# Optimization experiments

Measured on AMD Instinct MI355X. Metric: run time of the kernel, lower is better.

The kernel has to match this reference:

```python
import jax, jax.numpy as jnp
import numpy as np

D_MODEL = 1536
N_HEADS = 16
HEAD_DIM = D_MODEL // N_HEADS  # 96
NUM_BLOCKS = HEAD_DIM // 24    # 4


def generate_leech_kernel(dim=24):
    base = np.zeros((dim, dim), dtype=np.float32)
    for i in range(dim - 1):
        base[i, i] = 2.0
        base[i, i + 1] = 2.0
    base[-1, -1] = 2.0
    base[-1, 0] = -2.0
    q, _ = np.linalg.qr(base)
    return jnp.asarray(q.astype(np.float32))


def setup_inputs() -> dict:
    key = jax.random.key(0)
    k1, k2, k3 = jax.random.split(key, 3)
    x = jax.random.normal(k1, (2, 2048, D_MODEL), dtype=jnp.float32)
    # nn.Linear weights stored [out, in]; kept that layout, applied as x @ W.T
    w_qkv = jax.random.normal(k2, (3 * D_MODEL, D_MODEL), dtype=jnp.float32) * (D_MODEL ** -0.5)
    w_out = jax.random.normal(k3, (D_MODEL, D_MODEL), dtype=jnp.float32) * (D_MODEL ** -0.5)
    leech_kernel = generate_leech_kernel(24)
    return {"x": x, "w_qkv": w_qkv, "w_out": w_out, "leech_kernel": leech_kernel}


def _apply_kernel(t, kernel):
    # t: [b, h, s, head_dim] -> blockwise 24x24 rotation
    b, h, s, d = t.shape
    t = t.reshape(b, h, s, NUM_BLOCKS, 24)
    t = jnp.einsum('bhsni,ij->bhsnj', t, kernel)
    return t.reshape(b, h, s, d)


def reference(x, w_qkv, w_out, leech_kernel):
    bsz, steps, _ = x.shape
    qkv = x @ w_qkv.T  # [b, s, 3*d]
    qkv = qkv.reshape(bsz, steps, 3, N_HEADS, HEAD_DIM)
    qkv = jnp.transpose(qkv, (2, 0, 3, 1, 4))  # [3, b, h, s, hd]
    q, k, v = qkv[0], qkv[1], qkv[2]
    q = _apply_kernel(q, leech_kernel)
    k = _apply_kernel(k, leech_kernel)
    scale = HEAD_DIM ** -0.5
    scores = jnp.einsum('bhqd,bhkd->bhqk', q, k) * scale
    attn = jax.nn.softmax(scores, axis=-1)
    out = jnp.einsum('bhqk,bhkd->bhqd', attn, v)
    out = jnp.transpose(out, (0, 2, 1, 3)).reshape(bsz, steps, -1)
    return out @ w_out.T
```

## Files before the change

### kernel.cpp

```cpp
#include <hip/hip_runtime.h>
#include <cmath>

#define D_MODEL 1536
#define N_HEADS 16
#define HEAD_DIM 96
#define SEQ 2048
#define BATCH 2
#define M_TOTAL 4096
#define N_QKV 4608
#define QK_LOG2E 0.14724449f

typedef unsigned short ushort_t;
typedef __attribute__((ext_vector_type(8))) short bf16x8;
typedef __attribute__((ext_vector_type(4))) float f32x4;

static __device__ __forceinline__ ushort_t f2bf(float f) {
    unsigned u = __builtin_bit_cast(unsigned, f);
    u += 0x7fffu + ((u >> 16) & 1u);
    return (ushort_t)(u >> 16);
}

static __device__ __forceinline__ unsigned pk2bf(float lo, float hi) {
#if __has_builtin(__builtin_amdgcn_cvt_pk_bf16_f32)
    auto v = __builtin_amdgcn_cvt_pk_bf16_f32(lo, hi);
    return __builtin_bit_cast(unsigned, v);
#else
    return (unsigned)f2bf(lo) | ((unsigned)f2bf(hi) << 16);
#endif
}

static __device__ __forceinline__ float fast_exp2(float x) {
#if __has_builtin(__builtin_amdgcn_exp2f)
    return __builtin_amdgcn_exp2f(x);
#else
    return __expf(x * 0.69314718056f);
#endif
}

typedef const __attribute__((address_space(1))) unsigned int* gas_t;
typedef __attribute__((address_space(3))) unsigned int* las_t;
static __device__ __forceinline__ void gld_lds16(const void* g, void* l) {
    __builtin_amdgcn_global_load_lds((gas_t)g, (las_t)l, 16, 0, 0);
}

#define MFMA16(a, b, c) __builtin_amdgcn_mfma_f32_16x16x32_bf16(a, b, c, 0, 0, 0)

__global__ __launch_bounds__(256) void convert_f32_bf16(
    const float* __restrict__ in, ushort_t* __restrict__ out, int n)
{
    const int i = (blockIdx.x * 256 + threadIdx.x) * 4;
    if (i >= n) return;
    float4 v = *(const float4*)(in + i);
    ushort4 o;
    o.x = f2bf(v.x); o.y = f2bf(v.y); o.z = f2bf(v.z); o.w = f2bf(v.w);
    *(ushort4*)(out + i) = o;
}

__global__ __launch_bounds__(256) void prep_wqkv(
    const float* __restrict__ W, const float* __restrict__ Kern,
    ushort_t* __restrict__ Wb)
{
    __shared__ float Kl[576];
    const int t = threadIdx.x;
    for (int i = t; i < 576; i += 256) Kl[i] = Kern[i];
    __syncthreads();
    const int g = blockIdx.y;
    const int k = blockIdx.x * 256 + t;
    const float* src = W + (size_t)g * 24 * D_MODEL + k;
    ushort_t* dst = Wb + (size_t)g * 24 * D_MODEL + k;
    if (g < 128) {
        float in[24];
#pragma unroll
        for (int i = 0; i < 24; ++i) in[i] = src[(size_t)i * D_MODEL];
#pragma unroll
        for (int j = 0; j < 24; ++j) {
            float s = 0.f;
#pragma unroll
            for (int i = 0; i < 24; ++i) s = fmaf(in[i], Kl[i * 24 + j], s);
            dst[(size_t)j * D_MODEL] = f2bf(s);
        }
    } else {
#pragma unroll
        for (int i = 0; i < 24; ++i) dst[(size_t)i * D_MODEL] = f2bf(src[(size_t)i * D_MODEL]);
    }
}

__global__ __launch_bounds__(256, 4) void gemm_qkv_bf16(
    const ushort_t* __restrict__ X, const ushort_t* __restrict__ W,
    ushort_t* __restrict__ qb, ushort_t* __restrict__ kb, ushort_t* __restrict__ vtb)
{
    __shared__ ushort_t As[128 * 64];
    __shared__ ushort_t Bs[128 * 64];
    const int t = threadIdx.x;
    const int lane = t & 63, w = t >> 6;
    const int c = lane & 15, qd = lane >> 4;
    const int m0 = blockIdx.y * 128, n0 = blockIdx.x * 128;
    const int wr = (w >> 1) * 64, wc = (w & 1) * 64;
    const int lr = lane >> 3;
    const int lc = (lane & 7) ^ lr;
    const char* Xb = (const char*)X;
    const char* Wp = (const char*)W;
    const size_t rowb = 2 * D_MODEL;

    f32x4 acc[4][4];
#pragma unroll
    for (int i = 0; i < 4; ++i)
#pragma unroll
        for (int j = 0; j < 4; ++j) acc[i][j] = {0.f, 0.f, 0.f, 0.f};

    for (int k0 = 0; k0 < D_MODEL; k0 += 64) {
        __syncthreads();
#pragma unroll
        for (int j = 0; j < 4; ++j) {
            const int g = w * 4 + j;
            const int row = g * 8 + lr;
            gld_lds16(Xb + (size_t)(m0 + row) * rowb + k0 * 2 + lc * 16,
                      (char*)As + g * 1024);
            gld_lds16(Wp + (size_t)(n0 + row) * rowb + k0 * 2 + lc * 16,
                      (char*)Bs + g * 1024);
        }
        __syncthreads();
#pragma unroll
        for (int kc = 0; kc < 2; ++kc) {
            const int sx = ((kc * 4 + qd) ^ (c & 7)) * 16;
            bf16x8 af[4], bfr[4];
#pragma unroll
            for (int i = 0; i < 4; ++i)
                af[i] = *(const bf16x8*)((const char*)As + (wr + i * 16 + c) * 128 + sx);
#pragma unroll
            for (int j = 0; j < 4; ++j)
                bfr[j] = *(const bf16x8*)((const char*)Bs + (wc + j * 16 + c) * 128 + sx);
#pragma unroll
            for (int i = 0; i < 4; ++i)
#pragma unroll
                for (int j = 0; j < 4; ++j)
                    acc[i][j] = MFMA16(af[i], bfr[j], acc[i][j]);
        }
    }
#pragma unroll
    for (int j = 0; j < 4; ++j) {
        const int n = n0 + wc + j * 16 + c;
        const int which = n / D_MODEL;
        const int rem = n % D_MODEL;
        const int head = rem / HEAD_DIM;
        const int d = rem % HEAD_DIM;
        if (which < 2) {
            ushort_t* dst = which == 0 ? qb : kb;
            const float sc2 = which == 0 ? QK_LOG2E : 1.0f;
#pragma unroll
            for (int i = 0; i < 4; ++i)
#pragma unroll
                for (int r = 0; r < 4; ++r) {
                    const int m = m0 + wr + i * 16 + qd * 4 + r;
                    const int b_ = m >> 11, s_ = m & (SEQ - 1);
                    dst[((size_t)(b_ * N_HEADS + head) * SEQ + s_) * HEAD_DIM + d] =
                        f2bf(acc[i][j][r] * sc2);
                }
        } else {
            const int b_ = m0 >> 11;
            const int sb = (m0 & (SEQ - 1)) + wr + qd * 4;
            ushort_t* dstv = vtb + ((size_t)(b_ * N_HEADS + head) * HEAD_DIM + d) * SEQ;
#pragma unroll
            for (int i = 0; i < 4; ++i) {
                ushort4 o4;
                o4.x = f2bf(acc[i][j][0]); o4.y = f2bf(acc[i][j][1]);
                o4.z = f2bf(acc[i][j][2]); o4.w = f2bf(acc[i][j][3]);
                *(ushort4*)&dstv[sb + i * 16] = o4;
            }
        }
    }
}

__global__ __launch_bounds__(256, 4) void gemm_out_bf16(
    const ushort_t* __restrict__ A, const ushort_t* __restrict__ W,
    float* __restrict__ C)
{
    __shared__ ushort_t As[128 * 64];
    __shared__ ushort_t Bs[128 * 64];
    const int t = threadIdx.x;
    const int lane = t & 63, w = t >> 6;
    const int c = lane & 15, qd = lane >> 4;
    const int m0 = blockIdx.y * 128, n0 = blockIdx.x * 128;
    const int wr = (w >> 1) * 64, wc = (w & 1) * 64;
    const int lr = lane >> 3;
    const int lc = (lane & 7) ^ lr;
    const char* Ab = (const char*)A;
    const char* Wp = (const char*)W;
    const size_t rowb = 2 * D_MODEL;

    f32x4 acc[4][4];
#pragma unroll
    for (int i = 0; i < 4; ++i)
#pragma unroll
        for (int j = 0; j < 4; ++j) acc[i][j] = {0.f, 0.f, 0.f, 0.f};

    for (int k0 = 0; k0 < D_MODEL; k0 += 64) {
        __syncthreads();
#pragma unroll
        for (int j = 0; j < 4; ++j) {
            const int g = w * 4 + j;
            const int row = g * 8 + lr;
            gld_lds16(Ab + (size_t)(m0 + row) * rowb + k0 * 2 + lc * 16,
                      (char*)As + g * 1024);
            gld_lds16(Wp + (size_t)(n0 + row) * rowb + k0 * 2 + lc * 16,
                      (char*)Bs + g * 1024);
        }
        __syncthreads();
#pragma unroll
        for (int kc = 0; kc < 2; ++kc) {
            const int sx = ((kc * 4 + qd) ^ (c & 7)) * 16;
            bf16x8 af[4], bfr[4];
#pragma unroll
            for (int i = 0; i < 4; ++i)
                af[i] = *(const bf16x8*)((const char*)As + (wr + i * 16 + c) * 128 + sx);
#pragma unroll
            for (int j = 0; j < 4; ++j)
                bfr[j] = *(const bf16x8*)((const char*)Bs + (wc + j * 16 + c) * 128 + sx);
#pragma unroll
            for (int i = 0; i < 4; ++i)
#pragma unroll
                for (int j = 0; j < 4; ++j)
                    acc[i][j] = MFMA16(af[i], bfr[j], acc[i][j]);
        }
    }
#pragma unroll
    for (int i = 0; i < 4; ++i)
#pragma unroll
        for (int j = 0; j < 4; ++j)
#pragma unroll
            for (int r = 0; r < 4; ++r)
                C[(size_t)(m0 + wr + i * 16 + qd * 4 + r) * D_MODEL + n0 + wc + j * 16 + c] =
                    acc[i][j][r];
}

__global__ __launch_bounds__(256, 1) void flash_bf16(
    const ushort_t* __restrict__ Q, const ushort_t* __restrict__ K,
    const ushort_t* __restrict__ VT, ushort_t* __restrict__ attn)
{
    __shared__ ushort_t Ks[2][12 * 64 * 8];
    __shared__ ushort_t Vt[2][96 * 64];
    __shared__ ushort_t Ps[4][64 * 72];

    const int t = threadIdx.x;
    const int lane = t & 63, w = t >> 6;
    const int c = lane & 15, qd = lane >> 4;
    const int lr = lane >> 3;
    const int lc = (lane & 7) ^ lr;
    const int h = blockIdx.y, bb = blockIdx.z;
    const int q0 = blockIdx.x * 256;
    const size_t base = ((size_t)(bb * N_HEADS + h)) * SEQ * HEAD_DIM;
    const ushort_t* Qb = Q + base;
    const char* Kb = (const char*)(K + base);
    const ushort_t* VTb = VT + base;

    bf16x8 aq[4][3];
#pragma unroll
    for (int qi = 0; qi < 4; ++qi)
#pragma unroll
        for (int kc = 0; kc < 3; ++kc)
            aq[qi][kc] = *(const bf16x8*)(Qb +
                (size_t)(q0 + w * 64 + qi * 16 + c) * HEAD_DIM + kc * 32 + qd * 8);

    f32x4 oacc[6][4];
#pragma unroll
    for (int jd = 0; jd < 6; ++jd)
#pragma unroll
        for (int qi = 0; qi < 4; ++qi) oacc[jd][qi] = {0.f, 0.f, 0.f, 0.f};
    float lrow[4] = {0.f, 0.f, 0.f, 0.f};

    const int g0 = w * 3;
#define ISSUE_STAGE(buf, ktv)                                                   \
    {                                                                           \
        const char* kp = Kb + (size_t)(ktv) * 64 * 192;                         \
        _Pragma("unroll")                                                       \
        for (int jj = 0; jj < 3; ++jj) {                                        \
            const int g = g0 + jj;                                              \
            gld_lds16(kp + (size_t)lane * 192 + g * 16, (char*)Ks[buf] + g * 1024); \
        }                                                                       \
        _Pragma("unroll")                                                       \
        for (int jj = 0; jj < 3; ++jj) {                                        \
            const int g = g0 + jj;                                              \
            const int d = g * 8 + lr;                                           \
            gld_lds16((const char*)(VTb + (size_t)d * SEQ + (ktv) * 64 + lc * 8), \
                      (char*)Vt[buf] + g * 1024);                               \
        }                                                                       \
    }

    ISSUE_STAGE(0, 0)

    for (int kt = 0; kt < SEQ / 64; ++kt) {
        const int cur = kt & 1;
        __syncthreads();
        if (kt + 1 < SEQ / 64) ISSUE_STAGE(cur ^ 1, kt + 1)

        f32x4 sacc[4][4];
#pragma unroll
        for (int kti = 0; kti < 4; ++kti)
#pragma unroll
            for (int qi = 0; qi < 4; ++qi) sacc[kti][qi] = {0.f, 0.f, 0.f, 0.f};
#pragma unroll
        for (int kc = 0; kc < 3; ++kc) {
            bf16x8 ak[4];
#pragma unroll
            for (int kti = 0; kti < 4; ++kti)
                ak[kti] = *(const bf16x8*)&Ks[cur][((kc * 4 + qd) * 64 + kti * 16 + c) * 8];
#pragma unroll
            for (int kti = 0; kti < 4; ++kti)
#pragma unroll
                for (int qi = 0; qi < 4; ++qi)
                    sacc[kti][qi] = MFMA16(ak[kti], aq[qi][kc], sacc[kti][qi]);
        }

        float ls[4] = {0.f, 0.f, 0.f, 0.f};
#pragma unroll
        for (int kti = 0; kti < 4; ++kti)
#pragma unroll
            for (int qi = 0; qi < 4; ++qi) {
                const float p0 = fast_exp2(sacc[kti][qi][0]);
                const float p1 = fast_exp2(sacc[kti][qi][1]);
                const float p2 = fast_exp2(sacc[kti][qi][2]);
                const float p3 = fast_exp2(sacc[kti][qi][3]);
                uint2 pk;
                pk.x = pk2bf(p0, p1);
                pk.y = pk2bf(p2, p3);
                *(uint2*)&Ps[w][(qi * 16 + c) * 72 + kti * 16 + qd * 4] = pk;
                ls[qi] += (p0 + p1) + (p2 + p3);
            }
#pragma unroll
        for (int qi = 0; qi < 4; ++qi) {
            float v = ls[qi];
            v += __shfl_xor(v, 16, 64);
            v += __shfl_xor(v, 32, 64);
            lrow[qi] += v;
        }

#pragma unroll
        for (int kc = 0; kc < 2; ++kc) {
            bf16x8 bp[4];
#pragma unroll
            for (int qi = 0; qi < 4; ++qi)
                bp[qi] = *(const bf16x8*)&Ps[w][(qi * 16 + c) * 72 + kc * 32 + qd * 8];
#pragma unroll
            for (int jd = 0; jd < 6; ++jd) {
                const int sx = ((kc * 4 + qd) ^ (c & 7)) * 16;
                const bf16x8 av =
                    *(const bf16x8*)((const char*)Vt[cur] + (jd * 16 + c) * 128 + sx);
#pragma unroll
                for (int qi = 0; qi < 4; ++qi)
                    oacc[jd][qi] = MFMA16(av, bp[qi], oacc[jd][qi]);
            }
        }
    }
#undef ISSUE_STAGE

#pragma unroll
    for (int qi = 0; qi < 4; ++qi) {
        const float linv = 1.0f / lrow[qi];
        const int row = bb * SEQ + q0 + w * 64 + qi * 16 + c;
        ushort_t* dst = attn + (size_t)row * D_MODEL + h * HEAD_DIM + qd * 4;
#pragma unroll
        for (int jd = 0; jd < 6; ++jd) {
            ushort4 o4;
            o4.x = f2bf(oacc[jd][qi][0] * linv);
            o4.y = f2bf(oacc[jd][qi][1] * linv);
            o4.z = f2bf(oacc[jd][qi][2] * linv);
            o4.w = f2bf(oacc[jd][qi][3] * linv);
            *(ushort4*)(dst + jd * 16) = o4;
        }
    }
}


extern "C" void kernel_launch(void* const* d_in, const int* in_sizes, int n_in,
                              void* d_out, int out_size, void* d_ws, size_t ws_size,
                              hipStream_t stream)
{
    const float* x     = (const float*)d_in[0];
    const float* w_qkv = (const float*)d_in[1];
    const float* w_out = (const float*)d_in[2];
    const float* leech = (const float*)d_in[3];
    float* out = (float*)d_out;
    char* ws = (char*)d_ws;

    ushort_t* xb    = (ushort_t*)(ws);
    ushort_t* wqkvb = (ushort_t*)(ws + 12582912);
    ushort_t* woutb = (ushort_t*)(ws + 26738688);
    ushort_t* qb    = (ushort_t*)(ws + 31457280);
    ushort_t* kb    = (ushort_t*)(ws + 44040192);
    ushort_t* vtb   = (ushort_t*)(ws + 56623104);
    ushort_t* attnb = (ushort_t*)(ws + 69206016);

    convert_f32_bf16<<<6144, 256, 0, stream>>>(x, xb, M_TOTAL * D_MODEL);
    prep_wqkv<<<dim3(6, 192), 256, 0, stream>>>(w_qkv, leech, wqkvb);
    convert_f32_bf16<<<2304, 256, 0, stream>>>(w_out, woutb, D_MODEL * D_MODEL);

    gemm_qkv_bf16<<<dim3(N_QKV / 128, M_TOTAL / 128), 256, 0, stream>>>(
        xb, wqkvb, qb, kb, vtb);

    flash_bf16<<<dim3(SEQ / 256, N_HEADS, BATCH), 256, 0, stream>>>(
        qb, kb, vtb, attnb);

    gemm_out_bf16<<<dim3(D_MODEL / 128, M_TOTAL / 128), 256, 0, stream>>>(
        attnb, woutb, out);
}
```

Before: 315.8 us.

## Split flash attention key tiles across warp pairs and merge partial outputs

Each block now handles 128 queries instead of 256. Pairs of warps share the same 64 queries and each warp processes half of every 64-key tile. This doubles the grid from 256 to 512 blocks and raises launch bounds to 2 blocks per CU, meant to improve occupancy on the many-CU device. At the end, partial outputs and row sums are reduced through shared memory, which adds an extra sync, shared-memory traffic and duplicated K/V loads per query.

```diff
diff --git a/kernel.cpp b/kernel.cpp
--- a/kernel.cpp
+++ b/kernel.cpp
@@ -233,25 +233,31 @@
                     acc[i][j][r];
 }
 
-__global__ __launch_bounds__(256, 1) void flash_bf16(
+#define PSTR 36
+
+__global__ __launch_bounds__(256, 2) void flash_bf16(
     const ushort_t* __restrict__ Q, const ushort_t* __restrict__ K,
     const ushort_t* __restrict__ VT, ushort_t* __restrict__ attn)
 {
-    __shared__ ushort_t Ks[2][12 * 64 * 8];
-    __shared__ ushort_t Vt[2][96 * 64];
-    __shared__ ushort_t Ps[4][64 * 72];
+    __shared__ __align__(16) char smem[67584];
+    ushort_t* KsBuf = (ushort_t*)smem;
+    ushort_t* VtBuf = (ushort_t*)(smem + 24576);
+    ushort_t* PsBuf = (ushort_t*)(smem + 49152);
 
     const int t = threadIdx.x;
     const int lane = t & 63, w = t >> 6;
+    const int qh = w & 1;
+    const int kh = w >> 1;
     const int c = lane & 15, qd = lane >> 4;
     const int lr = lane >> 3;
     const int lc = (lane & 7) ^ lr;
     const int h = blockIdx.y, bb = blockIdx.z;
-    const int q0 = blockIdx.x * 256;
+    const int q0 = blockIdx.x * 128;
     const size_t base = ((size_t)(bb * N_HEADS + h)) * SEQ * HEAD_DIM;
     const ushort_t* Qb = Q + base;
     const char* Kb = (const char*)(K + base);
     const ushort_t* VTb = VT + base;
+    ushort_t* Ps = PsBuf + w * (64 * PSTR);
 
     bf16x8 aq[4][3];
 #pragma unroll
@@ -259,7 +265,7 @@
 #pragma unroll
         for (int kc = 0; kc < 3; ++kc)
             aq[qi][kc] = *(const bf16x8*)(Qb +
-                (size_t)(q0 + w * 64 + qi * 16 + c) * HEAD_DIM + kc * 32 + qd * 8);
+                (size_t)(q0 + qh * 64 + qi * 16 + c) * HEAD_DIM + kc * 32 + qd * 8);
 
     f32x4 oacc[6][4];
 #pragma unroll
@@ -269,21 +275,23 @@
     float lrow[4] = {0.f, 0.f, 0.f, 0.f};
 
     const int g0 = w * 3;
-#define ISSUE_STAGE(buf, ktv)                                                   \
-    {                                                                           \
-        const char* kp = Kb + (size_t)(ktv) * 64 * 192;                         \
-        _Pragma("unroll")                                                       \
-        for (int jj = 0; jj < 3; ++jj) {                                        \
-            const int g = g0 + jj;                                              \
-            gld_lds16(kp + (size_t)lane * 192 + g * 16, (char*)Ks[buf] + g * 1024); \
-        }                                                                       \
-        _Pragma("unroll")                                                       \
-        for (int jj = 0; jj < 3; ++jj) {                                        \
-            const int g = g0 + jj;                                              \
-            const int d = g * 8 + lr;                                           \
-            gld_lds16((const char*)(VTb + (size_t)d * SEQ + (ktv) * 64 + lc * 8), \
-                      (char*)Vt[buf] + g * 1024);                               \
-        }                                                                       \
+#define ISSUE_STAGE(buf, ktv)                                                    \
+    {                                                                            \
+        const char* kp = Kb + (size_t)(ktv) * 64 * 192;                          \
+        char* ksb = (char*)KsBuf + (buf) * 12288;                                \
+        char* vtb2 = (char*)VtBuf + (buf) * 12288;                               \
+        _Pragma("unroll")                                                        \
+        for (int jj = 0; jj < 3; ++jj) {                                         \
+            const int g = g0 + jj;                                               \
+            gld_lds16(kp + (size_t)lane * 192 + g * 16, ksb + g * 1024);         \
+        }                                                                        \
+        _Pragma("unroll")                                                        \
+        for (int jj = 0; jj < 3; ++jj) {                                         \
+            const int g = g0 + jj;                                               \
+            const int d = g * 8 + lr;                                            \
+            gld_lds16((const char*)(VTb + (size_t)d * SEQ + (ktv) * 64 + lc * 8),\
+                      vtb2 + g * 1024);                                          \
+        }                                                                        \
     }
 
     ISSUE_STAGE(0, 0)
@@ -293,19 +301,23 @@
         __syncthreads();
         if (kt + 1 < SEQ / 64) ISSUE_STAGE(cur ^ 1, kt + 1)
 
-        f32x4 sacc[4][4];
-#pragma unroll
-        for (int kti = 0; kti < 4; ++kti)
+        const ushort_t* Ks = KsBuf + cur * (12 * 64 * 8);
+        const char* Vt = (const char*)VtBuf + cur * 12288;
+
+        f32x4 sacc[2][4];
+#pragma unroll
+        for (int kti = 0; kti < 2; ++kti)
 #pragma unroll
             for (int qi = 0; qi < 4; ++qi) sacc[kti][qi] = {0.f, 0.f, 0.f, 0.f};
 #pragma unroll
         for (int kc = 0; kc < 3; ++kc) {
-            bf16x8 ak[4];
-#pragma unroll
-            for (int kti = 0; kti < 4; ++kti)
-                ak[kti] = *(const bf16x8*)&Ks[cur][((kc * 4 + qd) * 64 + kti * 16 + c) * 8];
-#pragma unroll
-            for (int kti = 0; kti < 4; ++kti)
+            bf16x8 ak[2];
+#pragma unroll
+            for (int kti = 0; kti < 2; ++kti)
+                ak[kti] = *(const bf16x8*)
+                    &Ks[((kc * 4 + qd) * 64 + (kh * 2 + kti) * 16 + c) * 8];
+#pragma unroll
+            for (int kti = 0; kti < 2; ++kti)
 #pragma unroll
                 for (int qi = 0; qi < 4; ++qi)
                     sacc[kti][qi] = MFMA16(ak[kti], aq[qi][kc], sacc[kti][qi]);
@@ -313,7 +325,7 @@
 
         float ls[4] = {0.f, 0.f, 0.f, 0.f};
 #pragma unroll
-        for (int kti = 0; kti < 4; ++kti)
+        for (int kti = 0; kti < 2; ++kti)
 #pragma unroll
             for (int qi = 0; qi < 4; ++qi) {
                 const float p0 = fast_exp2(sacc[kti][qi][0]);
@@ -323,7 +335,7 @@
                 uint2 pk;
                 pk.x = pk2bf(p0, p1);
                 pk.y = pk2bf(p2, p3);
-                *(uint2*)&Ps[w][(qi * 16 + c) * 72 + kti * 16 + qd * 4] = pk;
+                *(uint2*)&Ps[(qi * 16 + c) * PSTR + kti * 16 + qd * 4] = pk;
                 ls[qi] += (p0 + p1) + (p2 + p3);
             }
 #pragma unroll
@@ -334,17 +346,15 @@
             lrow[qi] += v;
         }
 
-#pragma unroll
-        for (int kc = 0; kc < 2; ++kc) {
+        {
             bf16x8 bp[4];
 #pragma unroll
             for (int qi = 0; qi < 4; ++qi)
-                bp[qi] = *(const bf16x8*)&Ps[w][(qi * 16 + c) * 72 + kc * 32 + qd * 8];
+                bp[qi] = *(const bf16x8*)&Ps[(qi * 16 + c) * PSTR + qd * 8];
 #pragma unroll
             for (int jd = 0; jd < 6; ++jd) {
-                const int sx = ((kc * 4 + qd) ^ (c & 7)) * 16;
-                const bf16x8 av =
-                    *(const bf16x8*)((const char*)Vt[cur] + (jd * 16 + c) * 128 + sx);
+                const int sx = ((kh * 4 + qd) ^ (c & 7)) * 16;
+                const bf16x8 av = *(const bf16x8*)(Vt + (jd * 16 + c) * 128 + sx);
 #pragma unroll
                 for (int qi = 0; qi < 4; ++qi)
                     oacc[jd][qi] = MFMA16(av, bp[qi], oacc[jd][qi]);
@@ -353,19 +363,41 @@
     }
 #undef ISSUE_STAGE
 
-#pragma unroll
-    for (int qi = 0; qi < 4; ++qi) {
-        const float linv = 1.0f / lrow[qi];
-        const int row = bb * SEQ + q0 + w * 64 + qi * 16 + c;
-        ushort_t* dst = attn + (size_t)row * D_MODEL + h * HEAD_DIM + qd * 4;
-#pragma unroll
-        for (int jd = 0; jd < 6; ++jd) {
-            ushort4 o4;
-            o4.x = f2bf(oacc[jd][qi][0] * linv);
-            o4.y = f2bf(oacc[jd][qi][1] * linv);
-            o4.z = f2bf(oacc[jd][qi][2] * linv);
-            o4.w = f2bf(oacc[jd][qi][3] * linv);
-            *(ushort4*)(dst + jd * 16) = o4;
+    float* Or = (float*)smem;
+    float* lr2 = (float*)(smem + 51200);
+    __syncthreads();
+    if (kh == 1) {
+        float* orw = Or + qh * 6400;
+#pragma unroll
+        for (int qi = 0; qi < 4; ++qi)
+#pragma unroll
+            for (int jd = 0; jd < 6; ++jd)
+                *(float4*)&orw[(qi * 16 + c) * 100 + jd * 16 + qd * 4] =
+                    *(float4*)&oacc[jd][qi];
+        if (qd == 0)
+#pragma unroll
+            for (int qi = 0; qi < 4; ++qi)
+                lr2[qh * 64 + qi * 16 + c] = lrow[qi];
+    }
+    __syncthreads();
+    if (kh == 0) {
+        const float* orw = Or + qh * 6400;
+#pragma unroll
+        for (int qi = 0; qi < 4; ++qi) {
+            const float ltot = lrow[qi] + lr2[qh * 64 + qi * 16 + c];
+            const float linv = 1.0f / ltot;
+            const int row = bb * SEQ + q0 + qh * 64 + qi * 16 + c;
+            ushort_t* dst = attn + (size_t)row * D_MODEL + h * HEAD_DIM + qd * 4;
+#pragma unroll
+            for (int jd = 0; jd < 6; ++jd) {
+                const float4 po = *(const float4*)&orw[(qi * 16 + c) * 100 + jd * 16 + qd * 4];
+                ushort4 o4;
+                o4.x = f2bf((oacc[jd][qi][0] + po.x) * linv);
+                o4.y = f2bf((oacc[jd][qi][1] + po.y) * linv);
+                o4.z = f2bf((oacc[jd][qi][2] + po.z) * linv);
+                o4.w = f2bf((oacc[jd][qi][3] + po.w) * linv);
+                *(ushort4*)(dst + jd * 16) = o4;
+            }
         }
     }
 }
@@ -397,7 +429,7 @@
     gemm_qkv_bf16<<<dim3(N_QKV / 128, M_TOTAL / 128), 256, 0, stream>>>(
         xb, wqkvb, qb, kb, vtb);
 
-    flash_bf16<<<dim3(SEQ / 256, N_HEADS, BATCH), 256, 0, stream>>>(
+    flash_bf16<<<dim3(SEQ / 128, N_HEADS, BATCH), 256, 0, stream>>>(
         qb, kb, vtb, attnb);
 
     gemm_out_bf16<<<dim3(D_MODEL / 128, M_TOTAL / 128), 256, 0, stream>>>(
```

Result: no change. 310.0 us (-1.8%).
